# Optimization experiments

Measured on AMD Instinct MI355X. Metric: run time of the kernel, lower is better.

The kernel has to match this reference:

```python
import jax, jax.numpy as jnp
import numpy as np

EPS = 1e-5


def setup_inputs() -> dict:
    key = jax.random.key(0)
    ks = jax.random.split(key, 9)
    B, Cin, C, N, H, W = 8, 512, 256, 19, 128, 128
    return {
        "feat_ffm": jax.random.normal(ks[0], (B, Cin, H, W), dtype=jnp.float32),
        "coarse_x": jax.random.normal(ks[1], (B, N, H, W), dtype=jnp.float32),
        "conv1_w": jax.random.normal(ks[2], (C, Cin), dtype=jnp.float32) * (1.0 / np.sqrt(Cin)),
        "bn_gamma": jax.random.normal(ks[3], (C,), dtype=jnp.float32) * 0.1 + 1.0,
        "bn_beta": jax.random.normal(ks[4], (C,), dtype=jnp.float32) * 0.1,
        "bn_mean": jax.random.normal(ks[5], (C,), dtype=jnp.float32) * 0.1,
        "bn_var": jax.random.uniform(ks[6], (C,), dtype=jnp.float32, minval=0.5, maxval=1.5),
        "conv2_w": jax.random.normal(ks[7], (C, C), dtype=jnp.float32) * (1.0 / np.sqrt(C)),
        "conv2_b": jax.random.normal(ks[8], (C,), dtype=jnp.float32) * 0.01,
    }


def reference(feat_ffm, coarse_x, conv1_w, bn_gamma, bn_beta, bn_mean, bn_var, conv2_w, conv2_b):
    # conv1: 1x1 conv (no bias) + BatchNorm (eval) + ReLU; Dropout2d is identity in eval.
    feat = jnp.einsum('bihw,oi->bohw', feat_ffm, conv1_w)          # [B,C,H,W]
    scale = bn_gamma / jnp.sqrt(bn_var + EPS)                      # [C]
    bias = bn_beta - bn_mean * scale
    feat = jax.nn.relu(feat * scale[None, :, None, None] + bias[None, :, None, None])

    B, N, H, W = coarse_x.shape
    C = feat.shape[1]
    q = coarse_x.reshape(B, N, H * W)                              # proj_query [B,N,HW]
    k = feat.reshape(B, C, H * W)                                  # proj_key^T is [B,HW,C]
    energy = jnp.einsum('bns,bcs->bnc', q, k)                      # [B,N,C]
    attn = jax.nn.softmax(energy, axis=-1)                         # softmax over C
    out = jnp.einsum('bnc,bns->bcs', attn, q)                      # attn^T @ value -> [B,C,HW]
    out = out.reshape(B, C, H, W)
    out = jnp.einsum('bihw,oi->bohw', out, conv2_w) + conv2_b[None, :, None, None]
    return out
```

## Files before the change

### kernel.cpp

```cpp
#include <hip/hip_runtime.h>

typedef __attribute__((ext_vector_type(8))) _Float16 f16x8;
typedef __attribute__((ext_vector_type(4))) float f32x4;
typedef __attribute__((ext_vector_type(2))) float f32x2;

#define MFMA16(A, Bv, Cv) __builtin_amdgcn_mfma_f32_16x16x32_f16(A, Bv, Cv, 0, 0, 0)

#define NB 8
#define CIN 512
#define NC 256
#define NQ 19

#define WS_WH 0
#define WS_WL 262144
#define WS_W2T 524288
#define WS_BIAS 786432
#define WS_M 787456

__global__ __launch_bounds__(256) void k_prep(
    const float* __restrict__ w1, const float* __restrict__ gamma,
    const float* __restrict__ beta, const float* __restrict__ mean,
    const float* __restrict__ var, const float* __restrict__ w2,
    char* __restrict__ ws) {
  _Float16* wh = (_Float16*)(ws + WS_WH);
  _Float16* wl = (_Float16*)(ws + WS_WL);
  float* w2t = (float*)(ws + WS_W2T);
  float* bias = (float*)(ws + WS_BIAS);
  const int bid = blockIdx.x, t = threadIdx.x;
  if (bid < 128) {
    for (int u = 0; u < 4; ++u) {
      int e = bid * 1024 + u * 256 + t;
      int j = e & 7, l6 = (e >> 3) & 63, mfq = (e >> 9) & 15, kk = e >> 13;
      int c = mfq * 16 + (l6 & 15);
      int k = kk * 32 + (l6 >> 4) * 8 + j;
      float sc = gamma[c] / sqrtf(var[c] + 1e-5f);
      float wf = w1[c * 512 + k] * sc * 32.0f;
      _Float16 h = (_Float16)wf;
      wh[e] = h;
      wl[e] = (_Float16)(wf - (float)h);
    }
  } else if (bid < 192) {
    for (int u = 0; u < 4; ++u) {
      int e = (bid - 128) * 1024 + u * 256 + t;
      int i = e >> 8, o = e & 255;
      w2t[e] = w2[o * 256 + i];
    }
  } else {
    float sc = gamma[t] / sqrtf(var[t] + 1e-5f);
    bias[t] = beta[t] - mean[t] * sc;
  }
}

__global__ __launch_bounds__(256, 4) void k_conv1_energy(
    const float* __restrict__ x, const float* __restrict__ qx,
    const char* __restrict__ ws, float* __restrict__ part) {
  __shared__ __align__(16) char smem[21504];
  const int tid = threadIdx.x;
  const int l = tid & 63, wm = tid >> 6;
  const int a = l & 15, g = l >> 4;
  const int bid = blockIdx.x;
  const int sblk = bid & 255, b = bid >> 8;
  const int s0 = sblk << 6;

  const f16x8* __restrict__ whv = (const f16x8*)(ws + WS_WH);
  const f16x8* __restrict__ wlv = (const f16x8*)(ws + WS_WL);
  {
    const float* bg = (const float*)(ws + WS_BIAS);
    ((float*)(smem + 20480))[tid] = bg[tid];
  }

  const int sigma = tid & 63;
  const int kc = wm;
  const float* __restrict__ xb = x + (((size_t)(b * CIN)) << 14) + s0 + sigma;

  f32x4 acc[4][4];
  const f32x4 zz = {0.f, 0.f, 0.f, 0.f};
  #pragma unroll
  for (int i = 0; i < 4; ++i)
    #pragma unroll
    for (int j = 0; j < 4; ++j) acc[i][j] = zz;

  float r[8];
  #pragma unroll
  for (int j = 0; j < 8; ++j)
    r[j] = xb[(size_t)(kc * 8 + j) << 14];

  #pragma unroll 2
  for (int kk = 0; kk < 16; ++kk) {
    f16x8 h0, l0;
    #pragma unroll
    for (int j = 0; j < 8; ++j) {
      float v = r[j] * 32.f;
      _Float16 h = (_Float16)v;
      h0[j] = h; l0[j] = (_Float16)(v - (float)h);
    }
    {
      char* wbase = smem + (kk & 1) * 10240;
      *(f16x8*)(wbase + sigma * 80 + kc * 16) = h0;
      *(f16x8*)(wbase + 5120 + sigma * 80 + kc * 16) = l0;
    }
    f16x8 ah[4], al[4];
    #pragma unroll
    for (int mf = 0; mf < 4; ++mf) {
      int aidx = (kk * 16 + wm * 4 + mf) * 64 + l;
      ah[mf] = whv[aidx];
      al[mf] = wlv[aidx];
    }
    if (kk < 15) {
      #pragma unroll
      for (int j = 0; j < 8; ++j)
        r[j] = xb[(size_t)((kk + 1) * 32 + kc * 8 + j) << 14];
    }
    asm volatile("s_waitcnt lgkmcnt(0)" ::: "memory");
    __builtin_amdgcn_sched_barrier(0);
    __builtin_amdgcn_s_barrier();
    __builtin_amdgcn_sched_barrier(0);
    const char* rb = smem + (kk & 1) * 10240;
    #pragma unroll
    for (int nf = 0; nf < 4; ++nf) {
      f16x8 bh = *(const f16x8*)(rb + (nf * 16 + a) * 80 + g * 16);
      f16x8 bl = *(const f16x8*)(rb + 5120 + (nf * 16 + a) * 80 + g * 16);
      #pragma unroll
      for (int mf = 0; mf < 4; ++mf) {
        acc[mf][nf] = MFMA16(ah[mf], bh, acc[mf][nf]);
        acc[mf][nf] = MFMA16(al[mf], bh, acc[mf][nf]);
        acc[mf][nf] = MFMA16(ah[mf], bl, acc[mf][nf]);
      }
    }
  }

  __syncthreads();

  {
    const float* blds = (const float*)(smem + 20480);
    #pragma unroll
    for (int mf = 0; mf < 4; ++mf)
      #pragma unroll
      for (int r4 = 0; r4 < 4; ++r4) {
        float bi = blds[wm * 64 + mf * 16 + g * 4 + r4];
        #pragma unroll
        for (int nf = 0; nf < 4; ++nf)
          acc[mf][nf][r4] = fmaxf(acc[mf][nf][r4] * (1.0f / 1024.0f) + bi, 0.f);
      }
  }

  float ea[19];
  #pragma unroll
  for (int n = 0; n < 19; ++n) ea[n] = 0.f;
  float* kvq = (float*)(smem + wm * 4352);
  const float* __restrict__ qb = qx + (((size_t)b * NQ) << 14) + s0;

  #pragma unroll
  for (int nf = 0; nf < 4; ++nf) {
    #pragma unroll
    for (int mf = 0; mf < 4; ++mf)
      *(f32x4*)&kvq[a * 68 + mf * 16 + g * 4] = acc[mf][nf];
    asm volatile("s_waitcnt lgkmcnt(0)" ::: "memory");
    __builtin_amdgcn_sched_barrier(0);
    #pragma unroll
    for (int spc = 0; spc < 4; ++spc) {
      float4 qv[19];
      #pragma unroll
      for (int n = 0; n < 19; ++n)
        qv[n] = *(const float4*)(qb + ((size_t)n << 14) + nf * 16 + spc * 4);
      #pragma unroll
      for (int sj = 0; sj < 4; ++sj) {
        float kv = kvq[(spc * 4 + sj) * 68 + l];
        #pragma unroll
        for (int n = 0; n < 19; ++n)
          ea[n] = fmaf(((const float*)&qv[n])[sj], kv, ea[n]);
      }
    }
  }

  float* pp = part + (size_t)bid * (NQ * 256) + wm * 64 + l;
  #pragma unroll
  for (int n = 0; n < 19; ++n)
    pp[n * 256] = ea[n];
}

__global__ __launch_bounds__(256) void k_softmax_m(
    const float* __restrict__ part, const char* __restrict__ ws,
    float* __restrict__ Mout) {
  const int bn = blockIdx.x;
  const int b = bn / 19, n = bn % 19;
  const int t = threadIdx.x;
  const float* __restrict__ w2t = (const float*)(ws + WS_W2T);
  float e = 0.f;
  const float* pp = part + ((size_t)(b * 256) * NQ + n) * 256 + t;
  for (int sb = 0; sb < 256; ++sb)
    e += pp[(size_t)sb * (NQ * 256)];
  __shared__ float sred[4];
  __shared__ float attn_lds[256];
  float m = e;
  #pragma unroll
  for (int d = 1; d < 64; d <<= 1) m = fmaxf(m, __shfl_xor(m, d, 64));
  if ((t & 63) == 0) sred[t >> 6] = m;
  __syncthreads();
  m = fmaxf(fmaxf(sred[0], sred[1]), fmaxf(sred[2], sred[3]));
  float p = __expf(e - m);
  float s = p;
  #pragma unroll
  for (int d = 1; d < 64; d <<= 1) s += __shfl_xor(s, d, 64);
  __syncthreads();
  if ((t & 63) == 0) sred[t >> 6] = s;
  __syncthreads();
  s = sred[0] + sred[1] + sred[2] + sred[3];
  attn_lds[t] = p / s;
  __syncthreads();
  float macc = 0.f;
  #pragma unroll 8
  for (int i = 0; i < 256; ++i)
    macc = fmaf(attn_lds[i], w2t[i * 256 + t], macc);
  Mout[(size_t)bn * 256 + t] = macc;
}

__global__ __launch_bounds__(256, 2) void k_out(
    const float* __restrict__ qx, const float* __restrict__ Mg,
    const float* __restrict__ b2, float* __restrict__ out) {
  const int bid = blockIdx.x;
  const int b = bid >> 6, sc = bid & 63;
  const int s0 = sc * 256;
  const int t = threadIdx.x;
  __shared__ float qlds[19 * 256];
  for (int idx = t; idx < 19 * 256; idx += 256) {
    int n = idx >> 8, s = idx & 255;
    qlds[idx] = qx[((size_t)(b * NQ + n) << 14) + s0 + s];
  }
  __syncthreads();
  const int tg = t >> 4, a2 = (t & 15) * 2;
  #pragma unroll 1
  for (int ocg = 0; ocg < 4; ++ocg) {
    float m[4][19];
    float bi[4];
    #pragma unroll
    for (int oj = 0; oj < 4; ++oj) {
      int o = (ocg * 4 + oj) * 16 + tg;
      bi[oj] = b2[o];
      #pragma unroll
      for (int n = 0; n < 19; ++n)
        m[oj][n] = Mg[((size_t)b * NQ + n) * 256 + o];
    }
    #pragma unroll 1
    for (int sp = 0; sp < 8; ++sp) {
      int s = sp * 32 + a2;
      f32x2 acc2[4];
      #pragma unroll
      for (int oj = 0; oj < 4; ++oj) { acc2[oj].x = bi[oj]; acc2[oj].y = bi[oj]; }
      #pragma unroll
      for (int n = 0; n < 19; ++n) {
        f32x2 q2 = *(const f32x2*)&qlds[n * 256 + s];
        #pragma unroll
        for (int oj = 0; oj < 4; ++oj) {
          acc2[oj].x = fmaf(m[oj][n], q2.x, acc2[oj].x);
          acc2[oj].y = fmaf(m[oj][n], q2.y, acc2[oj].y);
        }
      }
      #pragma unroll
      for (int oj = 0; oj < 4; ++oj) {
        int o = (ocg * 4 + oj) * 16 + tg;
        *(f32x2*)&out[((size_t)(b * NC + o) << 14) + s0 + s] = acc2[oj];
      }
    }
  }
}

extern "C" void kernel_launch(void* const* d_in, const int* in_sizes, int n_in,
                              void* d_out, int out_size, void* d_ws, size_t ws_size,
                              hipStream_t stream) {
  const float* x     = (const float*)d_in[0];
  const float* cx    = (const float*)d_in[1];
  const float* w1    = (const float*)d_in[2];
  const float* gamma = (const float*)d_in[3];
  const float* beta  = (const float*)d_in[4];
  const float* mean  = (const float*)d_in[5];
  const float* var   = (const float*)d_in[6];
  const float* w2    = (const float*)d_in[7];
  const float* b2    = (const float*)d_in[8];
  char* ws = (char*)d_ws;
  float* out = (float*)d_out;
  float* part = (float*)d_out;
  float* Mptr = (float*)(ws + WS_M);

  k_prep<<<193, 256, 0, stream>>>(w1, gamma, beta, mean, var, w2, ws);
  k_conv1_energy<<<2048, 256, 0, stream>>>(x, cx, ws, part);
  k_softmax_m<<<152, 256, 0, stream>>>(part, ws, Mptr);
  k_out<<<512, 256, 0, stream>>>(cx, Mptr, b2, out);
}
```

Baseline: 217.4 us.

## Retile conv1-energy kernel: 128 spatial per block, per-wave register B fragments

```diff
diff --git a/kernel.cpp b/kernel.cpp
--- a/kernel.cpp
+++ b/kernel.cpp
@@ -51,110 +51,105 @@
   }
 }
 
-__global__ __launch_bounds__(256, 4) void k_conv1_energy(
+__global__ __launch_bounds__(256, 2) void k_conv1_energy(
     const float* __restrict__ x, const float* __restrict__ qx,
     const char* __restrict__ ws, float* __restrict__ part) {
-  __shared__ __align__(16) char smem[21504];
+  __shared__ __align__(16) char smem[53248];
   const int tid = threadIdx.x;
-  const int l = tid & 63, wm = tid >> 6;
+  const int l = tid & 63, w = tid >> 6;
   const int a = l & 15, g = l >> 4;
+  const int h = w & 1;
   const int bid = blockIdx.x;
-  const int sblk = bid & 255, b = bid >> 8;
-  const int s0 = sblk << 6;
+  const int sblk = bid & 127, b = bid >> 7;
+  const int s0 = (sblk << 7) + ((w >> 1) << 6);
 
   const f16x8* __restrict__ whv = (const f16x8*)(ws + WS_WH);
   const f16x8* __restrict__ wlv = (const f16x8*)(ws + WS_WL);
+
+  const float* __restrict__ xb = x + (((size_t)(b * CIN)) << 14) + s0 + a;
+
+  f32x4 acc[8][4];
+  const f32x4 zz = {0.f, 0.f, 0.f, 0.f};
+  #pragma unroll
+  for (int i = 0; i < 8; ++i)
+    #pragma unroll
+    for (int j = 0; j < 4; ++j) acc[i][j] = zz;
+
+  float xr[4][8];
+  #pragma unroll
+  for (int nf = 0; nf < 4; ++nf)
+    #pragma unroll
+    for (int j = 0; j < 8; ++j)
+      xr[nf][j] = xb[((size_t)(g * 8 + j) << 14) + nf * 16];
+
+  f16x8 ah[2], al[2];
+
+  #pragma unroll 1
+  for (int kk = 0; kk < 16; ++kk) {
+    #pragma unroll
+    for (int m2 = 0; m2 < 2; ++m2) {
+      int aidx = (kk * 16 + h * 8 + m2) * 64 + l;
+      ah[m2] = whv[aidx];
+      al[m2] = wlv[aidx];
+    }
+    f16x8 bh[4], bl[4];
+    #pragma unroll
+    for (int nf = 0; nf < 4; ++nf)
+      #pragma unroll
+      for (int j = 0; j < 8; ++j) {
+        float v = xr[nf][j] * 32.f;
+        _Float16 hi = (_Float16)v;
+        bh[nf][j] = hi;
+        bl[nf][j] = (_Float16)(v - (float)hi);
+      }
+    if (kk < 15) {
+      #pragma unroll
+      for (int nf = 0; nf < 4; ++nf)
+        #pragma unroll
+        for (int j = 0; j < 8; ++j)
+          xr[nf][j] = xb[((size_t)((kk + 1) * 32 + g * 8 + j) << 14) + nf * 16];
+    }
+    #pragma unroll
+    for (int mf = 0; mf < 8; ++mf) {
+      f16x8 cah = ah[mf & 1], cal = al[mf & 1];
+      #pragma unroll
+      for (int nf = 0; nf < 4; ++nf) {
+        acc[mf][nf] = MFMA16(cah, bh[nf], acc[mf][nf]);
+        acc[mf][nf] = MFMA16(cal, bh[nf], acc[mf][nf]);
+        acc[mf][nf] = MFMA16(cah, bl[nf], acc[mf][nf]);
+      }
+      if (mf < 6) {
+        int aidx = (kk * 16 + h * 8 + mf + 2) * 64 + l;
+        ah[mf & 1] = whv[aidx];
+        al[mf & 1] = wlv[aidx];
+      }
+    }
+  }
+
   {
-    const float* bg = (const float*)(ws + WS_BIAS);
-    ((float*)(smem + 20480))[tid] = bg[tid];
-  }
-
-  const int sigma = tid & 63;
-  const int kc = wm;
-  const float* __restrict__ xb = x + (((size_t)(b * CIN)) << 14) + s0 + sigma;
-
-  f32x4 acc[4][4];
-  const f32x4 zz = {0.f, 0.f, 0.f, 0.f};
-  #pragma unroll
-  for (int i = 0; i < 4; ++i)
-    #pragma unroll
-    for (int j = 0; j < 4; ++j) acc[i][j] = zz;
-
-  float r[8];
-  #pragma unroll
-  for (int j = 0; j < 8; ++j)
-    r[j] = xb[(size_t)(kc * 8 + j) << 14];
-
-  #pragma unroll 2
-  for (int kk = 0; kk < 16; ++kk) {
-    f16x8 h0, l0;
-    #pragma unroll
-    for (int j = 0; j < 8; ++j) {
-      float v = r[j] * 32.f;
-      _Float16 h = (_Float16)v;
-      h0[j] = h; l0[j] = (_Float16)(v - (float)h);
-    }
-    {
-      char* wbase = smem + (kk & 1) * 10240;
-      *(f16x8*)(wbase + sigma * 80 + kc * 16) = h0;
-      *(f16x8*)(wbase + 5120 + sigma * 80 + kc * 16) = l0;
-    }
-    f16x8 ah[4], al[4];
-    #pragma unroll
-    for (int mf = 0; mf < 4; ++mf) {
-      int aidx = (kk * 16 + wm * 4 + mf) * 64 + l;
-      ah[mf] = whv[aidx];
-      al[mf] = wlv[aidx];
-    }
-    if (kk < 15) {
-      #pragma unroll
-      for (int j = 0; j < 8; ++j)
-        r[j] = xb[(size_t)((kk + 1) * 32 + kc * 8 + j) << 14];
-    }
-    asm volatile("s_waitcnt lgkmcnt(0)" ::: "memory");
-    __builtin_amdgcn_sched_barrier(0);
-    __builtin_amdgcn_s_barrier();
-    __builtin_amdgcn_sched_barrier(0);
-    const char* rb = smem + (kk & 1) * 10240;
-    #pragma unroll
-    for (int nf = 0; nf < 4; ++nf) {
-      f16x8 bh = *(const f16x8*)(rb + (nf * 16 + a) * 80 + g * 16);
-      f16x8 bl = *(const f16x8*)(rb + 5120 + (nf * 16 + a) * 80 + g * 16);
-      #pragma unroll
-      for (int mf = 0; mf < 4; ++mf) {
-        acc[mf][nf] = MFMA16(ah[mf], bh, acc[mf][nf]);
-        acc[mf][nf] = MFMA16(al[mf], bh, acc[mf][nf]);
-        acc[mf][nf] = MFMA16(ah[mf], bl, acc[mf][nf]);
-      }
-    }
-  }
-
-  __syncthreads();
-
-  {
-    const float* blds = (const float*)(smem + 20480);
-    #pragma unroll
-    for (int mf = 0; mf < 4; ++mf)
+    const float* __restrict__ biasg = (const float*)(ws + WS_BIAS);
+    #pragma unroll
+    for (int mf = 0; mf < 8; ++mf)
       #pragma unroll
       for (int r4 = 0; r4 < 4; ++r4) {
-        float bi = blds[wm * 64 + mf * 16 + g * 4 + r4];
+        float bi = biasg[h * 128 + mf * 16 + g * 4 + r4];
         #pragma unroll
         for (int nf = 0; nf < 4; ++nf)
           acc[mf][nf][r4] = fmaxf(acc[mf][nf][r4] * (1.0f / 1024.0f) + bi, 0.f);
       }
   }
 
-  float ea[19];
-  #pragma unroll
-  for (int n = 0; n < 19; ++n) ea[n] = 0.f;
-  float* kvq = (float*)(smem + wm * 4352);
-  const float* __restrict__ qb = qx + (((size_t)b * NQ) << 14) + s0;
+  float ea0[19], ea1[19];
+  #pragma unroll
+  for (int n = 0; n < 19; ++n) { ea0[n] = 0.f; ea1[n] = 0.f; }
+  float* kvq = (float*)(smem + w * 8448);
+  const float* __restrict__ qb = qx + (((size_t)(b * NQ)) << 14) + s0;
 
   #pragma unroll
   for (int nf = 0; nf < 4; ++nf) {
     #pragma unroll
-    for (int mf = 0; mf < 4; ++mf)
-      *(f32x4*)&kvq[a * 68 + mf * 16 + g * 4] = acc[mf][nf];
+    for (int mf = 0; mf < 8; ++mf)
+      *(f32x4*)&kvq[a * 132 + mf * 16 + g * 4] = acc[mf][nf];
     asm volatile("s_waitcnt lgkmcnt(0)" ::: "memory");
     __builtin_amdgcn_sched_barrier(0);
     #pragma unroll
@@ -165,18 +160,35 @@
         qv[n] = *(const float4*)(qb + ((size_t)n << 14) + nf * 16 + spc * 4);
       #pragma unroll
       for (int sj = 0; sj < 4; ++sj) {
-        float kv = kvq[(spc * 4 + sj) * 68 + l];
+        float kv0 = kvq[(spc * 4 + sj) * 132 + l];
+        float kv1 = kvq[(spc * 4 + sj) * 132 + 64 + l];
         #pragma unroll
-        for (int n = 0; n < 19; ++n)
-          ea[n] = fmaf(((const float*)&qv[n])[sj], kv, ea[n]);
-      }
-    }
-  }
-
-  float* pp = part + (size_t)bid * (NQ * 256) + wm * 64 + l;
-  #pragma unroll
-  for (int n = 0; n < 19; ++n)
-    pp[n * 256] = ea[n];
+        for (int n = 0; n < 19; ++n) {
+          float qs = ((const float*)&qv[n])[sj];
+          ea0[n] = fmaf(qs, kv0, ea0[n]);
+          ea1[n] = fmaf(qs, kv1, ea1[n]);
+        }
+      }
+    }
+  }
+
+  float* comb = (float*)(smem + 33792 + h * 9728);
+  if (w >= 2) {
+    #pragma unroll
+    for (int n = 0; n < 19; ++n) {
+      comb[n * 128 + l] = ea0[n];
+      comb[n * 128 + 64 + l] = ea1[n];
+    }
+  }
+  __syncthreads();
+  if (w < 2) {
+    float* pp = part + (size_t)bid * (NQ * 256) + h * 128 + l;
+    #pragma unroll
+    for (int n = 0; n < 19; ++n) {
+      pp[n * 256]      = ea0[n] + comb[n * 128 + l];
+      pp[n * 256 + 64] = ea1[n] + comb[n * 128 + 64 + l];
+    }
+  }
 }
 
 __global__ __launch_bounds__(256) void k_softmax_m(
@@ -187,8 +199,8 @@
   const int t = threadIdx.x;
   const float* __restrict__ w2t = (const float*)(ws + WS_W2T);
   float e = 0.f;
-  const float* pp = part + ((size_t)(b * 256) * NQ + n) * 256 + t;
-  for (int sb = 0; sb < 256; ++sb)
+  const float* pp = part + ((size_t)(b * 128) * NQ + n) * 256 + t;
+  for (int sb = 0; sb < 128; ++sb)
     e += pp[(size_t)sb * (NQ * 256)];
   __shared__ float sred[4];
   __shared__ float attn_lds[256];
@@ -283,7 +295,7 @@
   float* Mptr = (float*)(ws + WS_M);
 
   k_prep<<<193, 256, 0, stream>>>(w1, gamma, beta, mean, var, w2, ws);
-  k_conv1_energy<<<2048, 256, 0, stream>>>(x, cx, ws, part);
+  k_conv1_energy<<<1024, 256, 0, stream>>>(x, cx, ws, part);
   k_softmax_m<<<152, 256, 0, stream>>>(part, ws, Mptr);
   k_out<<<512, 256, 0, stream>>>(cx, Mptr, b2, out);
 }
```

After: 238.8 us. 9.9% more time.

## Stage conv1 weights into LDS via async global_load_lds with ping-pong pipeline

Applied to the files above, without the earlier changes.

```diff
diff --git a/kernel.cpp b/kernel.cpp
--- a/kernel.cpp
+++ b/kernel.cpp
@@ -11,8 +11,7 @@
 #define NC 256
 #define NQ 19
 
-#define WS_WH 0
-#define WS_WL 262144
+#define WS_WA 0
 #define WS_W2T 524288
 #define WS_BIAS 786432
 #define WS_M 787456
@@ -22,22 +21,23 @@
     const float* __restrict__ beta, const float* __restrict__ mean,
     const float* __restrict__ var, const float* __restrict__ w2,
     char* __restrict__ ws) {
-  _Float16* wh = (_Float16*)(ws + WS_WH);
-  _Float16* wl = (_Float16*)(ws + WS_WL);
+  _Float16* wa = (_Float16*)(ws + WS_WA);
   float* w2t = (float*)(ws + WS_W2T);
   float* bias = (float*)(ws + WS_BIAS);
   const int bid = blockIdx.x, t = threadIdx.x;
   if (bid < 128) {
-    for (int u = 0; u < 4; ++u) {
-      int e = bid * 1024 + u * 256 + t;
-      int j = e & 7, l6 = (e >> 3) & 63, mfq = (e >> 9) & 15, kk = e >> 13;
-      int c = mfq * 16 + (l6 & 15);
-      int k = kk * 32 + (l6 >> 4) * 8 + j;
+    for (int u = 0; u < 8; ++u) {
+      int i = bid * 2048 + u * 256 + t;
+      int kk = i >> 14, r = i & 16383;
+      int half = r >> 13, q = r & 8191;
+      int mfq = q >> 9, s = q & 511;
+      int l = s >> 3, j = s & 7;
+      int c = mfq * 16 + (l & 15);
+      int k = kk * 32 + (l >> 4) * 8 + j;
       float sc = gamma[c] / sqrtf(var[c] + 1e-5f);
       float wf = w1[c * 512 + k] * sc * 32.0f;
       _Float16 h = (_Float16)wf;
-      wh[e] = h;
-      wl[e] = (_Float16)(wf - (float)h);
+      wa[i] = half ? (_Float16)(wf - (float)h) : h;
     }
   } else if (bid < 192) {
     for (int u = 0; u < 4; ++u) {
@@ -51,10 +51,10 @@
   }
 }
 
-__global__ __launch_bounds__(256, 4) void k_conv1_energy(
+__global__ __launch_bounds__(256, 3) void k_conv1_energy(
     const float* __restrict__ x, const float* __restrict__ qx,
     const char* __restrict__ ws, float* __restrict__ part) {
-  __shared__ __align__(16) char smem[21504];
+  __shared__ __align__(16) char smem[53248];
   const int tid = threadIdx.x;
   const int l = tid & 63, wm = tid >> 6;
   const int a = l & 15, g = l >> 4;
@@ -62,15 +62,8 @@
   const int sblk = bid & 255, b = bid >> 8;
   const int s0 = sblk << 6;
 
-  const f16x8* __restrict__ whv = (const f16x8*)(ws + WS_WH);
-  const f16x8* __restrict__ wlv = (const f16x8*)(ws + WS_WL);
-  {
-    const float* bg = (const float*)(ws + WS_BIAS);
-    ((float*)(smem + 20480))[tid] = bg[tid];
-  }
-
-  const int sigma = tid & 63;
-  const int kc = wm;
+  const char* __restrict__ wsA = ws + WS_WA;
+  const int sigma = tid & 63, kc = wm;
   const float* __restrict__ xb = x + (((size_t)(b * CIN)) << 14) + s0 + sigma;
 
   f32x4 acc[4][4];
@@ -80,75 +73,131 @@
     #pragma unroll
     for (int j = 0; j < 4; ++j) acc[i][j] = zz;
 
-  float r[8];
-  #pragma unroll
-  for (int j = 0; j < 8; ++j)
-    r[j] = xb[(size_t)(kc * 8 + j) << 14];
-
-  #pragma unroll 2
-  for (int kk = 0; kk < 16; ++kk) {
-    f16x8 h0, l0;
-    #pragma unroll
-    for (int j = 0; j < 8; ++j) {
-      float v = r[j] * 32.f;
-      _Float16 h = (_Float16)v;
-      h0[j] = h; l0[j] = (_Float16)(v - (float)h);
-    }
-    {
-      char* wbase = smem + (kk & 1) * 10240;
-      *(f16x8*)(wbase + sigma * 80 + kc * 16) = h0;
-      *(f16x8*)(wbase + 5120 + sigma * 80 + kc * 16) = l0;
-    }
+#define DMA_A(KK) do {                                                         \
+    const char* gsrc_ = wsA + (KK) * 32768 + (wm * 8) * 1024 + l * 16;         \
+    _Pragma("unroll") for (int ii = 0; ii < 8; ++ii)                           \
+      __builtin_amdgcn_global_load_lds(                                        \
+          (const unsigned int*)(gsrc_ + ii * 1024),                            \
+          (unsigned int*)&smem[(wm * 8 + ii) * 1024], 16, 0, 0);               \
+  } while (0)
+
+#define LOADX(XR, T)                                                           \
+    _Pragma("unroll") for (int j = 0; j < 8; ++j)                              \
+      (XR)[j] = xb[((size_t)((T) * 32 + kc * 8 + j)) << 14];
+
+#define CONVERT_WRITE(XR, WB) do {                                             \
+    f16x8 hv_, lv_;                                                            \
+    _Pragma("unroll") for (int j = 0; j < 8; ++j) {                            \
+      float v = (XR)[j] * 32.f; _Float16 hh = (_Float16)v;                     \
+      hv_[j] = hh; lv_[j] = (_Float16)(v - (float)hh); }                       \
+    *(f16x8*)((WB) + sigma * 80 + kc * 16) = hv_;                              \
+    *(f16x8*)((WB) + 5120 + sigma * 80 + kc * 16) = lv_;                       \
+  } while (0)
+
+#define AFRAG_READ(AH, AL)                                                     \
+    _Pragma("unroll") for (int mf = 0; mf < 4; ++mf) {                         \
+      (AH)[mf] = *(const f16x8*)&smem[(wm * 4 + mf) * 1024 + l * 16];          \
+      (AL)[mf] = *(const f16x8*)&smem[16384 + (wm * 4 + mf) * 1024 + l * 16];  \
+    }
+
+#define MFMA_PHASE(RB, AH, AL)                                                 \
+    _Pragma("unroll") for (int nf = 0; nf < 4; ++nf) {                         \
+      f16x8 bh = *(const f16x8*)((RB) + (nf * 16 + a) * 80 + g * 16);          \
+      f16x8 bl = *(const f16x8*)((RB) + 5120 + (nf * 16 + a) * 80 + g * 16);   \
+      _Pragma("unroll") for (int mf = 0; mf < 4; ++mf) {                       \
+        acc[mf][nf] = MFMA16((AH)[mf], bh, acc[mf][nf]);                       \
+        acc[mf][nf] = MFMA16((AL)[mf], bh, acc[mf][nf]);                       \
+        acc[mf][nf] = MFMA16((AH)[mf], bl, acc[mf][nf]);                       \
+      }                                                                        \
+    }
+
+  char* const buf0 = smem + 32768;
+  char* const buf1 = smem + 43008;
+  float xrE[8], xrO[8];
+
+  DMA_A(0);
+  LOADX(xrE, 0);
+  LOADX(xrO, 1);
+  asm volatile("s_waitcnt vmcnt(8)" ::: "memory");
+  CONVERT_WRITE(xrE, buf0);
+  asm volatile("s_waitcnt lgkmcnt(0)" ::: "memory");
+  __builtin_amdgcn_sched_barrier(0);
+  __builtin_amdgcn_s_barrier();
+  __builtin_amdgcn_sched_barrier(0);
+
+  #pragma unroll 1
+  for (int i = 0; i < 8; ++i) {
     f16x8 ah[4], al[4];
+    AFRAG_READ(ah, al);
+    asm volatile("s_waitcnt lgkmcnt(0)" ::: "memory");
+    __builtin_amdgcn_sched_barrier(0);
+    __builtin_amdgcn_s_barrier();
+    __builtin_amdgcn_sched_barrier(0);
+    DMA_A(2 * i + 1);
+    if (i < 7) {
+      LOADX(xrE, 2 * i + 2);
+      asm volatile("s_waitcnt vmcnt(16)" ::: "memory");
+    } else {
+      asm volatile("s_waitcnt vmcnt(8)" ::: "memory");
+    }
+    __builtin_amdgcn_sched_barrier(0);
+    CONVERT_WRITE(xrO, buf1);
+    __builtin_amdgcn_s_setprio(1);
+    MFMA_PHASE(buf0, ah, al);
+    __builtin_amdgcn_s_setprio(0);
+    if (i < 7) {
+      asm volatile("s_waitcnt vmcnt(8) lgkmcnt(0)" ::: "memory");
+    } else {
+      asm volatile("s_waitcnt vmcnt(0) lgkmcnt(0)" ::: "memory");
+    }
+    __builtin_amdgcn_sched_barrier(0);
+    __builtin_amdgcn_s_barrier();
+    __builtin_amdgcn_sched_barrier(0);
+    AFRAG_READ(ah, al);
+    asm volatile("s_waitcnt lgkmcnt(0)" ::: "memory");
+    __builtin_amdgcn_sched_barrier(0);
+    if (i < 7) {
+      __builtin_amdgcn_s_barrier();
+      __builtin_amdgcn_sched_barrier(0);
+      DMA_A(2 * i + 2);
+      LOADX(xrO, 2 * i + 3);
+      asm volatile("s_waitcnt vmcnt(16)" ::: "memory");
+      __builtin_amdgcn_sched_barrier(0);
+      CONVERT_WRITE(xrE, buf0);
+    }
+    __builtin_amdgcn_s_setprio(1);
+    MFMA_PHASE(buf1, ah, al);
+    __builtin_amdgcn_s_setprio(0);
+    if (i < 7) {
+      asm volatile("s_waitcnt vmcnt(8) lgkmcnt(0)" ::: "memory");
+      __builtin_amdgcn_sched_barrier(0);
+      __builtin_amdgcn_s_barrier();
+      __builtin_amdgcn_sched_barrier(0);
+    }
+  }
+
+  __syncthreads();
+
+  {
+    const float* __restrict__ biasg = (const float*)(ws + WS_BIAS);
     #pragma unroll
     for (int mf = 0; mf < 4; ++mf) {
-      int aidx = (kk * 16 + wm * 4 + mf) * 64 + l;
-      ah[mf] = whv[aidx];
-      al[mf] = wlv[aidx];
-    }
-    if (kk < 15) {
-      #pragma unroll
-      for (int j = 0; j < 8; ++j)
-        r[j] = xb[(size_t)((kk + 1) * 32 + kc * 8 + j) << 14];
-    }
-    asm volatile("s_waitcnt lgkmcnt(0)" ::: "memory");
-    __builtin_amdgcn_sched_barrier(0);
-    __builtin_amdgcn_s_barrier();
-    __builtin_amdgcn_sched_barrier(0);
-    const char* rb = smem + (kk & 1) * 10240;
-    #pragma unroll
-    for (int nf = 0; nf < 4; ++nf) {
-      f16x8 bh = *(const f16x8*)(rb + (nf * 16 + a) * 80 + g * 16);
-      f16x8 bl = *(const f16x8*)(rb + 5120 + (nf * 16 + a) * 80 + g * 16);
-      #pragma unroll
-      for (int mf = 0; mf < 4; ++mf) {
-        acc[mf][nf] = MFMA16(ah[mf], bh, acc[mf][nf]);
-        acc[mf][nf] = MFMA16(al[mf], bh, acc[mf][nf]);
-        acc[mf][nf] = MFMA16(ah[mf], bl, acc[mf][nf]);
-      }
-    }
-  }
-
-  __syncthreads();
-
-  {
-    const float* blds = (const float*)(smem + 20480);
-    #pragma unroll
-    for (int mf = 0; mf < 4; ++mf)
+      const float4 bq = *(const float4*)(biasg + wm * 64 + mf * 16 + g * 4);
       #pragma unroll
       for (int r4 = 0; r4 < 4; ++r4) {
-        float bi = blds[wm * 64 + mf * 16 + g * 4 + r4];
+        float bi = ((const float*)&bq)[r4];
         #pragma unroll
         for (int nf = 0; nf < 4; ++nf)
           acc[mf][nf][r4] = fmaxf(acc[mf][nf][r4] * (1.0f / 1024.0f) + bi, 0.f);
       }
+    }
   }
 
   float ea[19];
   #pragma unroll
   for (int n = 0; n < 19; ++n) ea[n] = 0.f;
   float* kvq = (float*)(smem + wm * 4352);
-  const float* __restrict__ qb = qx + (((size_t)b * NQ) << 14) + s0;
+  const float* __restrict__ qb = qx + (((size_t)(b * NQ)) << 14) + s0;
 
   #pragma unroll
   for (int nf = 0; nf < 4; ++nf) {
```

Result: faster. 210.1 us (-3.3%).
